# Kernel tuning notes

Measured on AMD Instinct MI355X. Metric: run time of the kernel, lower is better.

Reference implementation:

```python
import jax, jax.numpy as jnp
import numpy as np
import math

B, H, S, D = 4, 16, 2048, 64

def setup_inputs() -> dict:
    key = jax.random.key(0)
    kq, kk, kv = jax.random.split(key, 3)
    Q = jax.random.normal(kq, (B, H, S, D), dtype=jnp.float32)
    K = jax.random.normal(kk, (B, H, S, D), dtype=jnp.float32)
    V = jax.random.normal(kv, (B, H, S, D), dtype=jnp.float32)
    # causal mask, broadcast to [B, H, S, S] as the module expects '... queries keys'
    causal = jnp.tril(jnp.ones((S, S), dtype=bool))
    mask = jnp.broadcast_to(causal, (B, H, S, S))
    return {"Q": Q, "K": K, "V": V, "mask": mask}

def reference(Q, K, V, mask):
    d_k = Q.shape[-1]
    # [B,H,S_q,S_k] scores
    qk = jnp.einsum('bhqd,bhkd->bhqk', Q, K) / math.sqrt(d_k)
    qk = jnp.where(mask, qk, -jnp.inf)
    sm = jax.nn.softmax(qk, axis=-1)
    return jnp.einsum('bhqk,bhkd->bhqd', sm, V)
```

## Files before the change

kernel.cpp:

```cpp
#include <hip/hip_runtime.h>

#define SEQ  2048
#define DH   64
#define QBLK 128
#define KBLK 64
#define NQB  (SEQ/QBLK)
#define NTIL (SEQ/KBLK)
#define THR  11.5f
#define KPAT(r) ((((r)&3)) + 8*((r)>>2))
#define WS_NEEDED ((size_t)2 * 64 * SEQ * DH * 2)

typedef short bf16x8 __attribute__((ext_vector_type(8)));
typedef float f32x16 __attribute__((ext_vector_type(16)));

union V4U { unsigned int w[4]; bf16x8 v; };

__device__ __forceinline__ short bfbits(float f) {
    unsigned int u = __float_as_uint(f);
    u += 0x7fff + ((u >> 16) & 1);
    return (short)(u >> 16);
}
__device__ __forceinline__ unsigned int cvtpk(float lo, float hi) {
    unsigned int r;
    asm("v_cvt_pk_bf16_f32 %0, %1, %2" : "=v"(r) : "v"(lo), "v"(hi));
    return r;
}
__device__ __forceinline__ int swz(int row, int col) {
    return row * 64 + (col ^ ((row & 7) << 3));
}

__global__ __launch_bounds__(256) void prep_kv(const float* __restrict__ Kg,
                                               const float* __restrict__ Vg,
                                               short* __restrict__ Kimg,
                                               short* __restrict__ Vimg) {
    __shared__ __align__(16) short Vt[64 * 64];
    const int tid = threadIdx.x;
    const int t   = blockIdx.x & (NTIL - 1);
    const int bh  = blockIdx.x / NTIL;
    const int kb  = t * KBLK;

    const float* Kb = Kg + (size_t)bh * SEQ * DH;
    const float* Vb = Vg + (size_t)bh * SEQ * DH;
    short* kim = Kimg + ((size_t)bh * NTIL + t) * 4096;
    short* vim = Vimg + ((size_t)bh * NTIL + t) * 4096;

    {
        const int kr = tid >> 2, dc = tid & 3;
        const float* src = Kb + (size_t)(kb + kr) * DH + dc * 16;
        const float4 a0 = *reinterpret_cast<const float4*>(src);
        const float4 a1 = *reinterpret_cast<const float4*>(src + 4);
        const float4 a2 = *reinterpret_cast<const float4*>(src + 8);
        const float4 a3 = *reinterpret_cast<const float4*>(src + 12);
        V4U u0, u1;
        u0.w[0] = cvtpk(a0.x, a0.y); u0.w[1] = cvtpk(a0.z, a0.w);
        u0.w[2] = cvtpk(a1.x, a1.y); u0.w[3] = cvtpk(a1.z, a1.w);
        u1.w[0] = cvtpk(a2.x, a2.y); u1.w[1] = cvtpk(a2.z, a2.w);
        u1.w[2] = cvtpk(a3.x, a3.y); u1.w[3] = cvtpk(a3.z, a3.w);
        const int sub = kr >> 5, row = kr & 31;
        *reinterpret_cast<bf16x8*>(&kim[dc * 1024 +   0 + sub * 256 + row * 8]) = u0.v;
        *reinterpret_cast<bf16x8*>(&kim[dc * 1024 + 512 + sub * 256 + row * 8]) = u1.v;
    }
    {
        const int vk = tid & 63, vd0 = (tid >> 6) * 16;
        const float* src = Vb + (size_t)(kb + vk) * DH + vd0;
        const float4 b0 = *reinterpret_cast<const float4*>(src);
        const float4 b1 = *reinterpret_cast<const float4*>(src + 4);
        const float4 b2 = *reinterpret_cast<const float4*>(src + 8);
        const float4 b3 = *reinterpret_cast<const float4*>(src + 12);
        const float vv[16] = {b0.x,b0.y,b0.z,b0.w, b1.x,b1.y,b1.z,b1.w,
                              b2.x,b2.y,b2.z,b2.w, b3.x,b3.y,b3.z,b3.w};
        #pragma unroll
        for (int i = 0; i < 16; ++i)
            Vt[swz(vd0 + i, vk)] = bfbits(vv[i]);
    }
    __syncthreads();
    #pragma unroll
    for (int c = 0; c < 2; ++c) {
        const int flat  = tid * 16 + c * 8;
        const int combo = flat >> 9;
        const int d     = (flat >> 3) & 63;
        const int col   = (combo >> 1) * 16 + (combo & 1) * 8;
        *reinterpret_cast<bf16x8*>(&vim[flat]) =
            *reinterpret_cast<const bf16x8*>(&Vt[swz(d, col)]);
    }
}

__device__ __forceinline__ void load_qfrags(const float* Qb, int q, int h, float SC,
                                            bf16x8 (&qb)[4]) {
    const float* qp = Qb + (size_t)q * DH + h * 8;
    #pragma unroll
    for (int dc = 0; dc < 4; ++dc) {
        const float4 a = *reinterpret_cast<const float4*>(qp + dc * 16);
        const float4 b = *reinterpret_cast<const float4*>(qp + dc * 16 + 4);
        V4U u;
        u.w[0] = cvtpk(a.x * SC, a.y * SC);
        u.w[1] = cvtpk(a.z * SC, a.w * SC);
        u.w[2] = cvtpk(b.x * SC, b.y * SC);
        u.w[3] = cvtpk(b.z * SC, b.w * SC);
        qb[dc] = u.v;
    }
}

__device__ __forceinline__ f32x16 qk32g(const short* __restrict__ kt_, int sub, int ql, int h,
                                        const bf16x8 (&qb)[4]) {
    f32x16 s;
    #pragma unroll
    for (int i = 0; i < 16; ++i) s[i] = 0.f;
    bf16x8 kf[4];
    #pragma unroll
    for (int dc = 0; dc < 4; ++dc)
        kf[dc] = *reinterpret_cast<const bf16x8*>(&kt_[dc * 1024 + h * 512 + sub * 256 + ql * 8]);
    __builtin_amdgcn_s_setprio(1);
    #pragma unroll
    for (int dc = 0; dc < 4; ++dc)
        s = __builtin_amdgcn_mfma_f32_32x32x16_bf16(kf[dc], qb[dc], s, 0, 0, 0);
    __builtin_amdgcn_s_setprio(0);
    return s;
}

__device__ __forceinline__ void sm_pack(f32x16& s0, f32x16& s1, bool v2,
                                        int kb, int qw, int q, int h,
                                        float& m, float& lsum,
                                        f32x16& o0, f32x16& o1, bf16x8 (&pa)[4]) {
    if (kb + 31 > qw) {
        #pragma unroll
        for (int r = 0; r < 16; ++r)
            if (kb + KPAT(r) + 4 * h > q) s0[r] = -1e30f;
    }
    if (v2 && (kb + 63 > qw)) {
        #pragma unroll
        for (int r = 0; r < 16; ++r)
            if (kb + 32 + KPAT(r) + 4 * h > q) s1[r] = -1e30f;
    }
    float mx = s0[0];
    #pragma unroll
    for (int r = 1; r < 16; ++r) mx = fmaxf(mx, s0[r]);
    if (v2) {
        #pragma unroll
        for (int r = 0; r < 16; ++r) mx = fmaxf(mx, s1[r]);
    }
    if (!__all(mx <= m + THR)) {
        mx = fmaxf(mx, __shfl_xor(mx, 32));
        const float mn  = fmaxf(m, mx);
        const float scl = __builtin_amdgcn_exp2f(m - mn);
        m = mn;
        lsum *= scl;
        #pragma unroll
        for (int r = 0; r < 16; ++r) {
            const float sr = __shfl(scl, KPAT(r) + 4 * h);
            o0[r] *= sr; o1[r] *= sr;
        }
    }
    #pragma unroll
    for (int r = 0; r < 16; ++r) { s0[r] = __builtin_amdgcn_exp2f(s0[r] - m); lsum += s0[r]; }
    #pragma unroll
    for (int oct = 0; oct < 2; ++oct) {
        const unsigned int A0 = cvtpk(s0[oct*8+0], s0[oct*8+1]);
        const unsigned int A1 = cvtpk(s0[oct*8+2], s0[oct*8+3]);
        const unsigned int B0 = cvtpk(s0[oct*8+4], s0[oct*8+5]);
        const unsigned int B1 = cvtpk(s0[oct*8+6], s0[oct*8+7]);
        const unsigned int t0 = h ? A0 : B0, t1 = h ? A1 : B1;
        const unsigned int r0 = (unsigned int)__shfl_xor((int)t0, 32);
        const unsigned int r1 = (unsigned int)__shfl_xor((int)t1, 32);
        V4U u;
        u.w[0] = h ? r0 : A0; u.w[1] = h ? r1 : A1;
        u.w[2] = h ? B0 : r0; u.w[3] = h ? B1 : r1;
        pa[oct] = u.v;
    }
    if (v2) {
        #pragma unroll
        for (int r = 0; r < 16; ++r) { s1[r] = __builtin_amdgcn_exp2f(s1[r] - m); lsum += s1[r]; }
        #pragma unroll
        for (int oct = 0; oct < 2; ++oct) {
            const unsigned int A0 = cvtpk(s1[oct*8+0], s1[oct*8+1]);
            const unsigned int A1 = cvtpk(s1[oct*8+2], s1[oct*8+3]);
            const unsigned int B0 = cvtpk(s1[oct*8+4], s1[oct*8+5]);
            const unsigned int B1 = cvtpk(s1[oct*8+6], s1[oct*8+7]);
            const unsigned int t0 = h ? A0 : B0, t1 = h ? A1 : B1;
            const unsigned int r0 = (unsigned int)__shfl_xor((int)t0, 32);
            const unsigned int r1 = (unsigned int)__shfl_xor((int)t1, 32);
            V4U u;
            u.w[0] = h ? r0 : A0; u.w[1] = h ? r1 : A1;
            u.w[2] = h ? B0 : r0; u.w[3] = h ? B1 : r1;
            pa[2 + oct] = u.v;
        }
    }
}

__device__ __forceinline__ void epilogue_store(float* Ob, int qw, int h, int ql,
                                               const f32x16& o0, const f32x16& o1,
                                               float lsum) {
    lsum += __shfl_xor(lsum, 32);
    const float inv = 1.0f / lsum;
    #pragma unroll
    for (int r = 0; r < 16; ++r) {
        const float ir  = __shfl(inv, KPAT(r) + 4 * h);
        const size_t row = (size_t)(qw + KPAT(r) + 4 * h);
        Ob[row * DH + ql]      = o0[r] * ir;
        Ob[row * DH + 32 + ql] = o1[r] * ir;
    }
}

__global__ __launch_bounds__(64, 3) void attn_fwd(const float* __restrict__ Qg,
                                                  const short* __restrict__ Kimg,
                                                  const short* __restrict__ Vimg,
                                                  float* __restrict__ Og) {
    const int lane = threadIdx.x;
    const int h    = lane >> 5;
    const int ql   = lane & 31;

    const int xcd  = blockIdx.x & 7;
    const int rest = blockIdx.x >> 3;
    const int bh   = xcd * 8 + (rest & 7);
    const int widx = rest >> 3;
    const int qblk = (NQB - 1) - (widx >> 2);
    const int w    = widx & 3;

    const float* Qb   = Qg + (size_t)bh * SEQ * DH;
    const short* kimg = Kimg + (size_t)bh * NTIL * 4096;
    const short* vimg = Vimg + (size_t)bh * NTIL * 4096;
    float*       Ob   = Og + (size_t)bh * SEQ * DH;

    const float SC = 0.125f * 1.44269504f;

    const int qw   = qblk * QBLK + w * 32;
    const int q    = qw + ql;
    const int kend = qw + 32;
    const int nt   = (kend + KBLK - 1) / KBLK;

    bf16x8 qb[4];
    load_qfrags(Qb, q, h, SC, qb);

    f32x16 o0, o1;
    #pragma unroll
    for (int i = 0; i < 16; ++i) { o0[i] = 0.f; o1[i] = 0.f; }
    float m = -1e30f, lsum = 0.f;

    for (int t = 0; t < nt; ++t) {
        const int kb = t * KBLK;
        const bool v2 = (kb + 32 < kend);
        const short* kt_ = kimg + (size_t)t * 4096;
        const short* vt_ = vimg + (size_t)t * 4096;

        f32x16 s0 = qk32g(kt_, 0, ql, h, qb);
        f32x16 s1;
        if (v2) s1 = qk32g(kt_, 1, ql, h, qb);

        bf16x8 vf[8];
        #pragma unroll
        for (int kt = 0; kt < 4; ++kt) {
            vf[kt]     = *reinterpret_cast<const bf16x8*>(&vt_[kt * 1024 + h * 512 +       ql * 8]);
            vf[4 + kt] = *reinterpret_cast<const bf16x8*>(&vt_[kt * 1024 + h * 512 + 256 + ql * 8]);
        }

        bf16x8 pa[4];
        sm_pack(s0, s1, v2, kb, qw, q, h, m, lsum, o0, o1, pa);

        __builtin_amdgcn_s_setprio(1);
        #pragma unroll
        for (int kt = 0; kt < 2; ++kt) {
            o0 = __builtin_amdgcn_mfma_f32_32x32x16_bf16(pa[kt], vf[kt],     o0, 0, 0, 0);
            o1 = __builtin_amdgcn_mfma_f32_32x32x16_bf16(pa[kt], vf[4 + kt], o1, 0, 0, 0);
        }
        if (v2) {
            #pragma unroll
            for (int kt = 2; kt < 4; ++kt) {
                o0 = __builtin_amdgcn_mfma_f32_32x32x16_bf16(pa[kt], vf[kt],     o0, 0, 0, 0);
                o1 = __builtin_amdgcn_mfma_f32_32x32x16_bf16(pa[kt], vf[4 + kt], o1, 0, 0, 0);
            }
        }
        __builtin_amdgcn_s_setprio(0);
    }

    epilogue_store(Ob, qw, h, ql, o0, o1, lsum);
}

__global__ __launch_bounds__(256) void attn_fwd_fb(const float* __restrict__ Qg,
                                                   const float* __restrict__ Kg,
                                                   const float* __restrict__ Vg,
                                                   float* __restrict__ Og) {
    __shared__ __align__(16) short Ks[64 * 64];
    __shared__ __align__(16) short Vt[64 * 64];

    const int tid  = threadIdx.x;
    const int w    = tid >> 6;
    const int lane = tid & 63;
    const int h    = lane >> 5;
    const int ql   = lane & 31;

    const int qblk = blockIdx.x & (NQB - 1);
    const int bh   = blockIdx.x / NQB;
    const int q0   = qblk * QBLK;
    const int qw   = q0 + w * 32;
    const int q    = qw + ql;

    const float* Qb = Qg + (size_t)bh * SEQ * DH;
    const float* Kb = Kg + (size_t)bh * SEQ * DH;
    const float* Vb = Vg + (size_t)bh * SEQ * DH;
    float*       Ob = Og + (size_t)bh * SEQ * DH;

    const float SC = 0.125f * 1.44269504f;

    const int skr  = tid >> 2;
    const int sd0  = (tid & 3) * 16;
    const int svk  = tid & 63;
    const int svd0 = (tid >> 6) * 16;

    bf16x8 qb[4];
    load_qfrags(Qb, q, h, SC, qb);

    f32x16 o0, o1;
    #pragma unroll
    for (int i = 0; i < 16; ++i) { o0[i] = 0.f; o1[i] = 0.f; }
    float m = -1e30f, lsum = 0.f;

    const int kend = qw + 32;
    const int nt   = (q0 + QBLK) / KBLK;

    for (int t = 0; t < nt; ++t) {
        const int kb = t * KBLK;
        __syncthreads();
        {
            const float* src = Kb + (size_t)(kb + skr) * DH + sd0;
            const float4 a0 = *reinterpret_cast<const float4*>(src);
            const float4 a1 = *reinterpret_cast<const float4*>(src + 4);
            const float4 a2 = *reinterpret_cast<const float4*>(src + 8);
            const float4 a3 = *reinterpret_cast<const float4*>(src + 12);
            V4U u0, u1;
            u0.w[0] = cvtpk(a0.x, a0.y); u0.w[1] = cvtpk(a0.z, a0.w);
            u0.w[2] = cvtpk(a1.x, a1.y); u0.w[3] = cvtpk(a1.z, a1.w);
            u1.w[0] = cvtpk(a2.x, a2.y); u1.w[1] = cvtpk(a2.z, a2.w);
            u1.w[2] = cvtpk(a3.x, a3.y); u1.w[3] = cvtpk(a3.z, a3.w);
            *reinterpret_cast<bf16x8*>(&Ks[swz(skr, sd0)])     = u0.v;
            *reinterpret_cast<bf16x8*>(&Ks[swz(skr, sd0 + 8)]) = u1.v;

            const float* vsrc = Vb + (size_t)(kb + svk) * DH + svd0;
            const float4 b0 = *reinterpret_cast<const float4*>(vsrc);
            const float4 b1 = *reinterpret_cast<const float4*>(vsrc + 4);
            const float4 b2 = *reinterpret_cast<const float4*>(vsrc + 8);
            const float4 b3 = *reinterpret_cast<const float4*>(vsrc + 12);
            const float vv[16] = {b0.x,b0.y,b0.z,b0.w, b1.x,b1.y,b1.z,b1.w,
                                  b2.x,b2.y,b2.z,b2.w, b3.x,b3.y,b3.z,b3.w};
            #pragma unroll
            for (int i = 0; i < 16; ++i)
                Vt[swz(svd0 + i, svk)] = bfbits(vv[i]);
        }
        __syncthreads();

        if (kb < kend) {
            const bool v2 = (kb + 32 < kend);
            f32x16 s0, s1;
            {
                bf16x8 kf[4];
                #pragma unroll
                for (int i = 0; i < 16; ++i) s0[i] = 0.f;
                #pragma unroll
                for (int dc = 0; dc < 4; ++dc)
                    kf[dc] = *reinterpret_cast<const bf16x8*>(&Ks[swz(ql, dc * 16 + h * 8)]);
                #pragma unroll
                for (int dc = 0; dc < 4; ++dc)
                    s0 = __builtin_amdgcn_mfma_f32_32x32x16_bf16(kf[dc], qb[dc], s0, 0, 0, 0);
                if (v2) {
                    #pragma unroll
                    for (int i = 0; i < 16; ++i) s1[i] = 0.f;
                    #pragma unroll
                    for (int dc = 0; dc < 4; ++dc)
                        kf[dc] = *reinterpret_cast<const bf16x8*>(&Ks[swz(32 + ql, dc * 16 + h * 8)]);
                    #pragma unroll
                    for (int dc = 0; dc < 4; ++dc)
                        s1 = __builtin_amdgcn_mfma_f32_32x32x16_bf16(kf[dc], qb[dc], s1, 0, 0, 0);
                }
            }
            bf16x8 pa[4];
            sm_pack(s0, s1, v2, kb, qw, q, h, m, lsum, o0, o1, pa);
            #pragma unroll
            for (int kt = 0; kt < 2; ++kt) {
                const bf16x8 vb0 = *reinterpret_cast<const bf16x8*>(&Vt[swz(ql,      kt * 16 + h * 8)]);
                const bf16x8 vb1 = *reinterpret_cast<const bf16x8*>(&Vt[swz(32 + ql, kt * 16 + h * 8)]);
                o0 = __builtin_amdgcn_mfma_f32_32x32x16_bf16(pa[kt], vb0, o0, 0, 0, 0);
                o1 = __builtin_amdgcn_mfma_f32_32x32x16_bf16(pa[kt], vb1, o1, 0, 0, 0);
            }
            if (v2) {
                #pragma unroll
                for (int kt = 2; kt < 4; ++kt) {
                    const bf16x8 vb0 = *reinterpret_cast<const bf16x8*>(&Vt[swz(ql,      kt * 16 + h * 8)]);
                    const bf16x8 vb1 = *reinterpret_cast<const bf16x8*>(&Vt[swz(32 + ql, kt * 16 + h * 8)]);
                    o0 = __builtin_amdgcn_mfma_f32_32x32x16_bf16(pa[kt], vb0, o0, 0, 0, 0);
                    o1 = __builtin_amdgcn_mfma_f32_32x32x16_bf16(pa[kt], vb1, o1, 0, 0, 0);
                }
            }
        }
    }

    epilogue_store(Ob, qw, h, ql, o0, o1, lsum);
}

extern "C" void kernel_launch(void* const* d_in, const int* in_sizes, int n_in,
                              void* d_out, int out_size, void* d_ws, size_t ws_size,
                              hipStream_t stream) {
    const float* Q = (const float*)d_in[0];
    const float* K = (const float*)d_in[1];
    const float* V = (const float*)d_in[2];
    float* O = (float*)d_out;

    if (ws_size >= WS_NEEDED) {
        short* Kimg = (short*)d_ws;
        short* Vimg = Kimg + (size_t)64 * NTIL * 4096;
        prep_kv<<<dim3(64 * NTIL), 256, 0, stream>>>(K, V, Kimg, Vimg);
        attn_fwd<<<dim3(64 * 64), 64, 0, stream>>>(Q, Kimg, Vimg, O);
    } else {
        attn_fwd_fb<<<dim3(64 * NQB), 256, 0, stream>>>(Q, K, V, O);
    }
}
```

Baseline: 79.15 us.

## Process two 32-row query tiles per wave to reuse K/V fragments

Each single-wave block now handles 64 query rows as two 32-row tiles, A and B, instead of one 32-row tile. Each loaded K and V fragment is therefore used by twice as many MFMAs, halving global/L2 fragment loads per unit of work. The grid shrinks from 4096 to 2048 blocks. Launch bounds drop to 2 waves per SIMD to allow the extra accumulator registers, which cuts occupancy and latency hiding.

```diff
diff --git a/kernel.cpp b/kernel.cpp
--- a/kernel.cpp
+++ b/kernel.cpp
@@ -101,23 +101,6 @@
     }
 }
 
-__device__ __forceinline__ f32x16 qk32g(const short* __restrict__ kt_, int sub, int ql, int h,
-                                        const bf16x8 (&qb)[4]) {
-    f32x16 s;
-    #pragma unroll
-    for (int i = 0; i < 16; ++i) s[i] = 0.f;
-    bf16x8 kf[4];
-    #pragma unroll
-    for (int dc = 0; dc < 4; ++dc)
-        kf[dc] = *reinterpret_cast<const bf16x8*>(&kt_[dc * 1024 + h * 512 + sub * 256 + ql * 8]);
-    __builtin_amdgcn_s_setprio(1);
-    #pragma unroll
-    for (int dc = 0; dc < 4; ++dc)
-        s = __builtin_amdgcn_mfma_f32_32x32x16_bf16(kf[dc], qb[dc], s, 0, 0, 0);
-    __builtin_amdgcn_s_setprio(0);
-    return s;
-}
-
 __device__ __forceinline__ void sm_pack(f32x16& s0, f32x16& s1, bool v2,
                                         int kb, int qw, int q, int h,
                                         float& m, float& lsum,
@@ -201,7 +184,7 @@
     }
 }
 
-__global__ __launch_bounds__(64, 3) void attn_fwd(const float* __restrict__ Qg,
+__global__ __launch_bounds__(64, 2) void attn_fwd(const float* __restrict__ Qg,
                                                   const short* __restrict__ Kimg,
                                                   const short* __restrict__ Vimg,
                                                   float* __restrict__ Og) {
@@ -212,9 +195,10 @@
     const int xcd  = blockIdx.x & 7;
     const int rest = blockIdx.x >> 3;
     const int bh   = xcd * 8 + (rest & 7);
-    const int widx = rest >> 3;
-    const int qblk = (NQB - 1) - (widx >> 2);
-    const int w    = widx & 3;
+    const int u    = rest >> 3;
+    const int qblk = (NQB - 1) - (u >> 1);
+    const int half = u & 1;
+    const int qw64 = qblk * QBLK + half * 64;
 
     const float* Qb   = Qg + (size_t)bh * SEQ * DH;
     const short* kimg = Kimg + (size_t)bh * NTIL * 4096;
@@ -223,28 +207,63 @@
 
     const float SC = 0.125f * 1.44269504f;
 
-    const int qw   = qblk * QBLK + w * 32;
-    const int q    = qw + ql;
-    const int kend = qw + 32;
-    const int nt   = (kend + KBLK - 1) / KBLK;
-
-    bf16x8 qb[4];
-    load_qfrags(Qb, q, h, SC, qb);
-
-    f32x16 o0, o1;
-    #pragma unroll
-    for (int i = 0; i < 16; ++i) { o0[i] = 0.f; o1[i] = 0.f; }
-    float m = -1e30f, lsum = 0.f;
+    const int qwA = qw64,      qA = qwA + ql, kendA = qwA + 32;
+    const int qwB = qw64 + 32, qB = qwB + ql;
+    const int nt  = (qw64 + 64) / KBLK;
+
+    bf16x8 qbA[4], qbB[4];
+    load_qfrags(Qb, qA, h, SC, qbA);
+    load_qfrags(Qb, qB, h, SC, qbB);
+
+    f32x16 oA0, oA1, oB0, oB1;
+    #pragma unroll
+    for (int i = 0; i < 16; ++i) { oA0[i]=0.f; oA1[i]=0.f; oB0[i]=0.f; oB1[i]=0.f; }
+    float mA = -1e30f, lA = 0.f, mB = -1e30f, lB = 0.f;
 
     for (int t = 0; t < nt; ++t) {
         const int kb = t * KBLK;
-        const bool v2 = (kb + 32 < kend);
+        const bool v2A = (kb + 32 < kendA);
         const short* kt_ = kimg + (size_t)t * 4096;
         const short* vt_ = vimg + (size_t)t * 4096;
 
-        f32x16 s0 = qk32g(kt_, 0, ql, h, qb);
-        f32x16 s1;
-        if (v2) s1 = qk32g(kt_, 1, ql, h, qb);
+        f32x16 sA0, sA1, sB0, sB1;
+        {
+            bf16x8 kf[4];
+            #pragma unroll
+            for (int dc = 0; dc < 4; ++dc)
+                kf[dc] = *reinterpret_cast<const bf16x8*>(&kt_[dc * 1024 + h * 512 + ql * 8]);
+            #pragma unroll
+            for (int i = 0; i < 16; ++i) { sA0[i] = 0.f; sB0[i] = 0.f; }
+            __builtin_amdgcn_s_setprio(1);
+            #pragma unroll
+            for (int dc = 0; dc < 4; ++dc) {
+                sA0 = __builtin_amdgcn_mfma_f32_32x32x16_bf16(kf[dc], qbA[dc], sA0, 0, 0, 0);
+                sB0 = __builtin_amdgcn_mfma_f32_32x32x16_bf16(kf[dc], qbB[dc], sB0, 0, 0, 0);
+            }
+            __builtin_amdgcn_s_setprio(0);
+        }
+        {
+            bf16x8 kf[4];
+            #pragma unroll
+            for (int dc = 0; dc < 4; ++dc)
+                kf[dc] = *reinterpret_cast<const bf16x8*>(&kt_[dc * 1024 + h * 512 + 256 + ql * 8]);
+            #pragma unroll
+            for (int i = 0; i < 16; ++i) sB1[i] = 0.f;
+            if (v2A) {
+                #pragma unroll
+                for (int i = 0; i < 16; ++i) sA1[i] = 0.f;
+            }
+            __builtin_amdgcn_s_setprio(1);
+            #pragma unroll
+            for (int dc = 0; dc < 4; ++dc)
+                sB1 = __builtin_amdgcn_mfma_f32_32x32x16_bf16(kf[dc], qbB[dc], sB1, 0, 0, 0);
+            if (v2A) {
+                #pragma unroll
+                for (int dc = 0; dc < 4; ++dc)
+                    sA1 = __builtin_amdgcn_mfma_f32_32x32x16_bf16(kf[dc], qbA[dc], sA1, 0, 0, 0);
+            }
+            __builtin_amdgcn_s_setprio(0);
+        }
 
         bf16x8 vf[8];
         #pragma unroll
@@ -253,26 +272,39 @@
             vf[4 + kt] = *reinterpret_cast<const bf16x8*>(&vt_[kt * 1024 + h * 512 + 256 + ql * 8]);
         }
 
-        bf16x8 pa[4];
-        sm_pack(s0, s1, v2, kb, qw, q, h, m, lsum, o0, o1, pa);
-
-        __builtin_amdgcn_s_setprio(1);
-        #pragma unroll
-        for (int kt = 0; kt < 2; ++kt) {
-            o0 = __builtin_amdgcn_mfma_f32_32x32x16_bf16(pa[kt], vf[kt],     o0, 0, 0, 0);
-            o1 = __builtin_amdgcn_mfma_f32_32x32x16_bf16(pa[kt], vf[4 + kt], o1, 0, 0, 0);
-        }
-        if (v2) {
-            #pragma unroll
-            for (int kt = 2; kt < 4; ++kt) {
-                o0 = __builtin_amdgcn_mfma_f32_32x32x16_bf16(pa[kt], vf[kt],     o0, 0, 0, 0);
-                o1 = __builtin_amdgcn_mfma_f32_32x32x16_bf16(pa[kt], vf[4 + kt], o1, 0, 0, 0);
-            }
-        }
-        __builtin_amdgcn_s_setprio(0);
-    }
-
-    epilogue_store(Ob, qw, h, ql, o0, o1, lsum);
+        {
+            bf16x8 pa[4];
+            sm_pack(sA0, sA1, v2A, kb, qwA, qA, h, mA, lA, oA0, oA1, pa);
+            __builtin_amdgcn_s_setprio(1);
+            #pragma unroll
+            for (int kt = 0; kt < 2; ++kt) {
+                oA0 = __builtin_amdgcn_mfma_f32_32x32x16_bf16(pa[kt], vf[kt],     oA0, 0, 0, 0);
+                oA1 = __builtin_amdgcn_mfma_f32_32x32x16_bf16(pa[kt], vf[4 + kt], oA1, 0, 0, 0);
+            }
+            if (v2A) {
+                #pragma unroll
+                for (int kt = 2; kt < 4; ++kt) {
+                    oA0 = __builtin_amdgcn_mfma_f32_32x32x16_bf16(pa[kt], vf[kt],     oA0, 0, 0, 0);
+                    oA1 = __builtin_amdgcn_mfma_f32_32x32x16_bf16(pa[kt], vf[4 + kt], oA1, 0, 0, 0);
+                }
+            }
+            __builtin_amdgcn_s_setprio(0);
+        }
+        {
+            bf16x8 pa[4];
+            sm_pack(sB0, sB1, true, kb, qwB, qB, h, mB, lB, oB0, oB1, pa);
+            __builtin_amdgcn_s_setprio(1);
+            #pragma unroll
+            for (int kt = 0; kt < 4; ++kt) {
+                oB0 = __builtin_amdgcn_mfma_f32_32x32x16_bf16(pa[kt], vf[kt],     oB0, 0, 0, 0);
+                oB1 = __builtin_amdgcn_mfma_f32_32x32x16_bf16(pa[kt], vf[4 + kt], oB1, 0, 0, 0);
+            }
+            __builtin_amdgcn_s_setprio(0);
+        }
+    }
+
+    epilogue_store(Ob, qwA, h, ql, oA0, oA1, lA);
+    epilogue_store(Ob, qwB, h, ql, oB0, oB1, lB);
 }
 
 __global__ __launch_bounds__(256) void attn_fwd_fb(const float* __restrict__ Qg,
@@ -407,7 +439,7 @@
         short* Kimg = (short*)d_ws;
         short* Vimg = Kimg + (size_t)64 * NTIL * 4096;
         prep_kv<<<dim3(64 * NTIL), 256, 0, stream>>>(K, V, Kimg, Vimg);
-        attn_fwd<<<dim3(64 * 64), 64, 0, stream>>>(Q, Kimg, Vimg, O);
+        attn_fwd<<<dim3(2048), 64, 0, stream>>>(Q, Kimg, Vimg, O);
     } else {
         attn_fwd_fb<<<dim3(64 * NQB), 256, 0, stream>>>(Q, K, V, O);
     }
```

New measurement: 97.19 us. 1.23x slower.
